# Kernel optimization log

Hardware: AMD Instinct MI355X
Metric: run time of the kernel (lower is better)

The kernel has to match this reference:

```python
import jax, jax.numpy as jnp
import numpy as np

B, S, D, H = 1, 4096, 1024, 16
DH = D // H  # 64
SCALE = D ** 0.5  # original divides by input_dim**0.5, not head_dim**0.5


def setup_inputs() -> dict:
    key = jax.random.key(0)
    ks = jax.random.split(key, 11)
    s = lambda i, shape, sc=1.0: jax.random.normal(ks[i], shape, dtype=jnp.float32) * sc
    w_init = 1.0 / np.sqrt(D)
    return {
        "q": s(0, (B, S, D)),
        "k": s(1, (B, S, D)),
        "v": s(2, (B, S, D)),
        "Wq": s(3, (H, D, DH), w_init),
        "bq": jnp.zeros((H, DH), jnp.float32),
        "Wk": s(4, (H, D, DH), w_init),
        "bk": jnp.zeros((H, DH), jnp.float32),
        "Wv": s(5, (H, D, DH), w_init),
        "bv": jnp.zeros((H, DH), jnp.float32),
        "Wo": s(6, (D, D), w_init),
        "bo": jnp.zeros((D,), jnp.float32),
    }


def reference(q, k, v, Wq, bq, Wk, bk, Wv, bv, Wo, bo):
    # Per-head Dense projections, batched over heads: [B,S,D] x [H,D,dh] -> [B,H,S,dh]
    Q = jnp.einsum("bsd,hde->bhse", q, Wq) + bq[None, :, None, :]
    K = jnp.einsum("bsd,hde->bhse", k, Wk) + bk[None, :, None, :]
    V = jnp.einsum("bsd,hde->bhse", v, Wv) + bv[None, :, None, :]
    # Scaled dot-product attention; note scale = sqrt(input_dim) as in source
    scores = jnp.einsum("bhse,bhte->bhst", Q, K) / SCALE  # [B,H,S,S]
    attn = jax.nn.softmax(scores, axis=-1)
    out = jnp.einsum("bhst,bhte->bhse", attn, V)  # [B,H,S,dh]
    # Concat heads along feature dim (head order matches the Python loop)
    concat = out.transpose(0, 2, 1, 3).reshape(q.shape[0], q.shape[1], H * DH)
    return concat @ Wo + bo
```

## Files before the change

### kernel.cpp

```cpp
#include <hip/hip_runtime.h>
#include <hip/hip_bf16.h>

#define S_LEN 4096
#define D_MODEL 1024
#define NH 16
#define DHEAD 64
#define QSCALE 0.0450843293f

typedef __attribute__((ext_vector_type(8))) short short8;
typedef __attribute__((ext_vector_type(4))) float floatx4;

__device__ __forceinline__ unsigned short f2bf(float f) {
    unsigned int x = __float_as_uint(f);
    x += 0x7fffu + ((x >> 16) & 1u);
    return (unsigned short)(x >> 16);
}

__device__ __forceinline__ float exp2_fast(float x) {
    return __builtin_amdgcn_exp2f(x);
}

__device__ __forceinline__ void async_copy16(const unsigned short* g, unsigned short* l) {
    __builtin_amdgcn_global_load_lds(
        (const __attribute__((address_space(1))) void*)g,
        (__attribute__((address_space(3))) void*)l, 16, 0, 0);
}

__global__ __launch_bounds__(256) void prep_all(
    const float* __restrict__ q, const float* __restrict__ k,
    const float* __restrict__ v,
    const float* __restrict__ Wq, const float* __restrict__ Wk,
    const float* __restrict__ Wv, const float* __restrict__ Wo,
    unsigned short* __restrict__ dst, unsigned short* __restrict__ ws)
{
    __shared__ float L[64][65];
    const int tid = threadIdx.x;

    if (blockIdx.x < 6144) {
        long i = (long)(blockIdx.x * 256 + tid) * 8;
        int which = (int)(i >> 22);
        long off = i & ((1 << 22) - 1);
        const float* src = (which == 0) ? q : (which == 1) ? k : v;
        float4 f0 = *(const float4*)&src[off];
        float4 f1 = *(const float4*)&src[off + 4];
        uint4 o;
        o.x = (unsigned int)f2bf(f0.x) | ((unsigned int)f2bf(f0.y) << 16);
        o.y = (unsigned int)f2bf(f0.z) | ((unsigned int)f2bf(f0.w) << 16);
        o.z = (unsigned int)f2bf(f1.x) | ((unsigned int)f2bf(f1.y) << 16);
        o.w = (unsigned int)f2bf(f1.z) | ((unsigned int)f2bf(f1.w) << 16);
        *(uint4*)&dst[i] = o;
        return;
    }

    const int bx  = blockIdx.x - 6144;
    const int mat = bx >> 8;

    if (mat < 3) {
        const float* W = (mat == 0) ? Wq : (mat == 1) ? Wk : Wv;
        unsigned short* WT = ws + (size_t)mat * (1u << 20);
        int h  = (bx >> 4) & 15;
        int dt = bx & 15;
        #pragma unroll
        for (int i = 0; i < 16; i++) {
            int idx = i * 256 + tid;
            int dp = idx >> 6, e = idx & 63;
            L[e][dp] = W[h * 65536 + (dt * 64 + dp) * 64 + e];
        }
        __syncthreads();
        #pragma unroll
        for (int i = 0; i < 16; i++) {
            int idx = i * 256 + tid;
            int e = idx >> 6, dp = idx & 63;
            WT[(h * 64 + e) * 1024 + dt * 64 + dp] = f2bf(L[e][dp]);
        }
    } else {
        unsigned short* WoT = ws + (size_t)3 * (1u << 20);
        int rt = (bx >> 4) & 15;
        int ct = bx & 15;
        #pragma unroll
        for (int i = 0; i < 16; i++) {
            int idx = i * 256 + tid;
            int dp = idx >> 6, np = idx & 63;
            L[np][dp] = Wo[(rt * 64 + dp) * 1024 + ct * 64 + np];
        }
        __syncthreads();
        #pragma unroll
        for (int i = 0; i < 16; i++) {
            int idx = i * 256 + tid;
            int np = idx >> 6, dp = idx & 63;
            WoT[(ct * 64 + np) * 1024 + rt * 64 + dp] = f2bf(L[np][dp]);
        }
    }
}

#define GEMM_CORE(XPTR, WPTR)                                                   \
    for (int k0 = 0; k0 < D_MODEL; k0 += 64) {                                  \
        __syncthreads();                                                        \
        _Pragma("unroll")                                                       \
        for (int i = 0; i < 4; i++) {                                           \
            async_copy16(&XPTR[(size_t)(m0 + srow + i * 8) * D_MODEL + k0 + scol], \
                         &As[(wave * 32 + i * 8) * 64]);                        \
            async_copy16(&WPTR[(size_t)(n0 + srow + i * 8) * D_MODEL + k0 + scol], \
                         &Bs[(wave * 32 + i * 8) * 64]);                        \
        }                                                                       \
        __syncthreads();                                                        \
        _Pragma("unroll")                                                       \
        for (int ks = 0; ks < 2; ks++) {                                        \
            short8 af[4], bf[4];                                                \
            _Pragma("unroll")                                                   \
            for (int i = 0; i < 4; i++)                                         \
                af[i] = *(const short8*)&As[(wr * 64 + i * 16 + m) * 64 + ks * 32 + quad * 8]; \
            _Pragma("unroll")                                                   \
            for (int j = 0; j < 4; j++)                                         \
                bf[j] = *(const short8*)&Bs[(wc * 64 + j * 16 + m) * 64 + ks * 32 + quad * 8]; \
            _Pragma("unroll")                                                   \
            for (int i = 0; i < 4; i++) {                                       \
                _Pragma("unroll")                                               \
                for (int j = 0; j < 4; j++)                                     \
                    acc[i][j] = __builtin_amdgcn_mfma_f32_16x16x32_bf16(af[i], bf[j], acc[i][j], 0, 0, 0); \
            }                                                                   \
        }                                                                       \
    }

__global__ __launch_bounds__(256) void qkv_gemm(
    const unsigned short* __restrict__ Xbase, const unsigned short* __restrict__ WTbase,
    const float* __restrict__ bq, const float* __restrict__ bk,
    const float* __restrict__ bv,
    unsigned short* __restrict__ Qbuf, unsigned short* __restrict__ Kbuf,
    unsigned short* __restrict__ Vbuf)
{
    __shared__ __align__(16) unsigned short AB[2 * 128 * 64];
    unsigned short* As = AB;
    unsigned short* Bs = AB + 128 * 64;

    const int z = blockIdx.z;
    const unsigned short* X  = Xbase + (size_t)z * (4u << 20);
    const unsigned short* WT = WTbase + (size_t)z * (1u << 20);
    const float* bias = (z == 0) ? bq : (z == 1) ? bk : bv;

    const int n0 = blockIdx.x * 128;
    const int m0 = blockIdx.y * 128;
    const int tid = threadIdx.x, wave = tid >> 6, lane = tid & 63;
    const int m = lane & 15, quad = lane >> 4;
    const int wr = wave >> 1, wc = wave & 1;
    const int srow = wave * 32 + (lane >> 3);
    const int scol = (lane & 7) * 8;

    floatx4 acc[4][4];
    #pragma unroll
    for (int i = 0; i < 4; i++)
        #pragma unroll
        for (int j = 0; j < 4; j++) acc[i][j] = (floatx4){0.f, 0.f, 0.f, 0.f};

    GEMM_CORE(X, WT)

    if (z == 2) {
        #pragma unroll
        for (int j = 0; j < 4; j++) {
            int n = n0 + wc * 64 + j * 16 + m;
            int h = n >> 6, e = n & 63;
            float bvv = bias[n];
            #pragma unroll
            for (int i = 0; i < 4; i++) {
                int sbase = m0 + wr * 64 + i * 16 + quad * 4;
                ushort4 pk;
                pk.x = f2bf(acc[i][j][0] + bvv);
                pk.y = f2bf(acc[i][j][1] + bvv);
                pk.z = f2bf(acc[i][j][2] + bvv);
                pk.w = f2bf(acc[i][j][3] + bvv);
                *(ushort4*)&Vbuf[h * (DHEAD * S_LEN) + e * S_LEN + sbase] = pk;
            }
        }
        return;
    }

    const float scale = (z == 0) ? QSCALE : 1.0f;
    unsigned short* outp = (z == 0) ? Qbuf : Kbuf;
    __syncthreads();
    unsigned short* stage = wc ? Bs : As;
    #pragma unroll
    for (int j = 0; j < 4; j++) {
        int e = j * 16 + m;
        float bvv = bias[n0 + wc * 64 + e];
        #pragma unroll
        for (int i = 0; i < 4; i++) {
            int rbase = wr * 64 + i * 16 + quad * 4;
            #pragma unroll
            for (int r = 0; r < 4; r++) {
                int rowl = rbase + r;
                stage[rowl * 64 + (e ^ ((rowl & 7) << 3))] =
                    f2bf((acc[i][j][r] + bvv) * scale);
            }
        }
    }
    __syncthreads();
    const int h0 = n0 >> 6;
    const size_t base0 = (size_t)h0 * (S_LEN * DHEAD) + (size_t)m0 * DHEAD;
    const size_t base1 = base0 + (size_t)(S_LEN * DHEAD);
    #pragma unroll
    for (int s = 0; s < 4; s++) {
        int o = tid * 8 + s * 2048;
        int row = o >> 6, c0 = o & 63;
        int cs = c0 ^ ((row & 7) << 3);
        *(uint4*)&outp[base0 + o] = *(const uint4*)&As[row * 64 + cs];
        *(uint4*)&outp[base1 + o] = *(const uint4*)&Bs[row * 64 + cs];
    }
}

__global__ __launch_bounds__(256) void out_gemm(
    const unsigned short* __restrict__ Cbuf, const unsigned short* __restrict__ WoT,
    const float* __restrict__ bo, float* __restrict__ out)
{
    __shared__ __align__(16) unsigned short AB[2 * 128 * 64];
    unsigned short* As = AB;
    unsigned short* Bs = AB + 128 * 64;

    const int n0 = blockIdx.x * 128;
    const int m0 = blockIdx.y * 128;
    const int tid = threadIdx.x, wave = tid >> 6, lane = tid & 63;
    const int m = lane & 15, quad = lane >> 4;
    const int wr = wave >> 1, wc = wave & 1;
    const int srow = wave * 32 + (lane >> 3);
    const int scol = (lane & 7) * 8;

    floatx4 acc[4][4];
    #pragma unroll
    for (int i = 0; i < 4; i++)
        #pragma unroll
        for (int j = 0; j < 4; j++) acc[i][j] = (floatx4){0.f, 0.f, 0.f, 0.f};

    GEMM_CORE(Cbuf, WoT)

    __syncthreads();
    float* Fs = (float*)AB;
    #pragma unroll
    for (int half = 0; half < 2; half++) {
        if (wr == half) {
            #pragma unroll
            for (int j = 0; j < 4; j++) {
                int c = wc * 64 + j * 16 + m;
                float bvv = bo[n0 + c];
                #pragma unroll
                for (int i = 0; i < 4; i++) {
                    int rbase = i * 16 + quad * 4;
                    #pragma unroll
                    for (int r = 0; r < 4; r++) {
                        int rowl = rbase + r;
                        Fs[rowl * 128 + (c ^ ((rowl & 7) << 2))] = acc[i][j][r] + bvv;
                    }
                }
            }
        }
        __syncthreads();
        #pragma unroll
        for (int s = 0; s < 8; s++) {
            int o = tid * 4 + s * 1024;
            int row = o >> 7, c0 = o & 127;
            int cs = c0 ^ ((row & 7) << 2);
            *(float4*)&out[(size_t)(m0 + half * 64 + row) * D_MODEL + n0 + c0] =
                *(const float4*)&Fs[row * 128 + cs];
        }
        __syncthreads();
    }
}

__global__ __launch_bounds__(512) void attn_kernel(
    const unsigned short* __restrict__ Q, const unsigned short* __restrict__ K,
    const unsigned short* __restrict__ VT, unsigned short* __restrict__ concat)
{
    __shared__ __align__(16) unsigned char ldsraw[49152];
    unsigned short* lds16 = (unsigned short*)ldsraw;

    const int h  = blockIdx.y;
    const int q0 = blockIdx.x * 128;
    const unsigned short* Qh = Q  + h * (S_LEN * DHEAD);
    const unsigned short* Kh = K  + h * (S_LEN * DHEAD);
    const unsigned short* Vh = VT + h * (DHEAD * S_LEN);

    const int tid  = threadIdx.x;
    const int wave = tid >> 6;
    const int wt   = wave & 3;
    const int wq   = wave >> 2;
    const int lane = tid & 63;
    const int m    = lane & 15;
    const int quad = lane >> 4;
    const int swz  = (m & 7) << 3;
    const int lrow = lane >> 3;
    const int lcol = ((lane & 7) * 8) ^ (lrow << 3);

    unsigned short* Ps = lds16 + 16384;

    #pragma unroll
    for (int i = 0; i < 2; i++) {
        int c = 2 * wave + i;
        async_copy16(&Qh[(size_t)(q0 + 8 * c + lrow) * DHEAD + lcol], Ps + c * 512);
    }
    async_copy16(&Kh[(size_t)(8 * wave + lrow) * DHEAD + lcol], lds16 + wave * 512);
    async_copy16(&Vh[(size_t)(8 * wave + lrow) * S_LEN + lcol], lds16 + 8192 + wave * 512);
    asm volatile("s_waitcnt vmcnt(0)" ::: "memory");
    __builtin_amdgcn_s_barrier();

    short8 bq[4][2];
    #pragma unroll
    for (int qc = 0; qc < 4; qc++)
        #pragma unroll
        for (int ks = 0; ks < 2; ks++)
            bq[qc][ks] = *(const short8*)&Ps[(wq * 64 + qc * 16 + m) * 64 + ((ks * 32 + quad * 8) ^ swz)];
    __syncthreads();

    short8 vone;
    #pragma unroll
    for (int i = 0; i < 8; i++) vone[i] = (short)0x3F80;

    floatx4 O[4];
    #pragma unroll
    for (int nb = 0; nb < 4; nb++) O[nb] = (floatx4){0.f, 0.f, 0.f, 0.f};
    floatx4 Lacc = (floatx4){0.f, 0.f, 0.f, 0.f};

    for (int t0 = 0; t0 < S_LEN; t0 += 64) {
        const int cur = (t0 >> 6) & 1;
        unsigned short* Ksc = lds16 + cur * 4096;
        unsigned short* Vsc = lds16 + 8192 + cur * 4096;

        if (t0) {
            asm volatile("s_waitcnt vmcnt(0)" ::: "memory");
            __builtin_amdgcn_s_barrier();
        }
        if (t0 + 64 < S_LEN) {
            unsigned short* Ksn = lds16 + (cur ^ 1) * 4096;
            unsigned short* Vsn = lds16 + 8192 + (cur ^ 1) * 4096;
            async_copy16(&Kh[(size_t)(t0 + 64 + 8 * wave + lrow) * DHEAD + lcol],
                         Ksn + wave * 512);
            async_copy16(&Vh[(size_t)(8 * wave + lrow) * S_LEN + t0 + 64 + lcol],
                         Vsn + wave * 512);
        }

        floatx4 st[4];
        #pragma unroll
        for (int qc = 0; qc < 4; qc++) st[qc] = (floatx4){0.f, 0.f, 0.f, 0.f};
        #pragma unroll
        for (int ks = 0; ks < 2; ks++) {
            short8 a = *(const short8*)&Ksc[(wt * 16 + m) * 64 + ((ks * 32 + quad * 8) ^ swz)];
            __builtin_amdgcn_s_setprio(1);
            #pragma unroll
            for (int qc = 0; qc < 4; qc++)
                st[qc] = __builtin_amdgcn_mfma_f32_16x16x32_bf16(a, bq[qc][ks], st[qc], 0, 0, 0);
            __builtin_amdgcn_s_setprio(0);
        }

        #pragma unroll
        for (int qc = 0; qc < 4; qc++) {
            float p0 = exp2_fast(st[qc][0]);
            float p1 = exp2_fast(st[qc][1]);
            float p2 = exp2_fast(st[qc][2]);
            float p3 = exp2_fast(st[qc][3]);
            unsigned r0, r1;
            asm("v_cvt_pk_bf16_f32 %0, %1, %2" : "=v"(r0) : "v"(p0), "v"(p1));
            asm("v_cvt_pk_bf16_f32 %0, %1, %2" : "=v"(r1) : "v"(p2), "v"(p3));
            uint2 pk;
            pk.x = r0;
            pk.y = r1;
            *(uint2*)&Ps[(wq * 64 + qc * 16 + m) * 64 + ((wt * 16 + quad * 4) ^ swz)] = pk;
        }
        asm volatile("s_waitcnt lgkmcnt(0)" ::: "memory");
        __builtin_amdgcn_s_barrier();

        #pragma unroll
        for (int ks = 0; ks < 2; ks++) {
            short8 ap = *(const short8*)&Ps[(wave * 16 + m) * 64 + ((ks * 32 + quad * 8) ^ swz)];
            __builtin_amdgcn_s_setprio(1);
            #pragma unroll
            for (int nb = 0; nb < 4; nb++) {
                short8 bv = *(const short8*)&Vsc[(nb * 16 + m) * 64 + ((ks * 32 + quad * 8) ^ swz)];
                O[nb] = __builtin_amdgcn_mfma_f32_16x16x32_bf16(ap, bv, O[nb], 0, 0, 0);
            }
            Lacc = __builtin_amdgcn_mfma_f32_16x16x32_bf16(ap, vone, Lacc, 0, 0, 0);
            __builtin_amdgcn_s_setprio(0);
        }
    }

    float linv[4];
    #pragma unroll
    for (int r = 0; r < 4; r++) linv[r] = 1.0f / Lacc[r];

    #pragma unroll
    for (int nb = 0; nb < 4; nb++) {
        int e = nb * 16 + m;
        #pragma unroll
        for (int r = 0; r < 4; r++) {
            int s = q0 + wave * 16 + quad * 4 + r;
            concat[s * D_MODEL + h * DHEAD + e] = f2bf(O[nb][r] * linv[r]);
        }
    }
}

extern "C" void kernel_launch(void* const* d_in, const int* in_sizes, int n_in,
                              void* d_out, int out_size, void* d_ws, size_t ws_size,
                              hipStream_t stream) {
    const float* q  = (const float*)d_in[0];
    const float* k  = (const float*)d_in[1];
    const float* v  = (const float*)d_in[2];
    const float* Wq = (const float*)d_in[3];
    const float* bq = (const float*)d_in[4];
    const float* Wk = (const float*)d_in[5];
    const float* bk = (const float*)d_in[6];
    const float* Wv = (const float*)d_in[7];
    const float* bv = (const float*)d_in[8];
    const float* Wo = (const float*)d_in[9];
    const float* bo = (const float*)d_in[10];
    float* out = (float*)d_out;

    unsigned short* ws = (unsigned short*)d_ws;
    const size_t M1 = 1u << 20;
    unsigned short* WqT  = ws;
    unsigned short* WoT  = ws + 3 * M1;
    unsigned short* Qbuf = ws + 4 * M1;
    unsigned short* Kbuf = ws + 8 * M1;
    unsigned short* Vbuf = ws + 12 * M1;
    unsigned short* Cbuf = ws + 16 * M1;
    unsigned short* qb   = ws + 20 * M1;

    prep_all<<<7168, 256, 0, stream>>>(q, k, v, Wq, Wk, Wv, Wo, qb, ws);

    dim3 gq(8, 32, 3);
    qkv_gemm<<<gq, 256, 0, stream>>>(qb, WqT, bq, bk, bv, Qbuf, Kbuf, Vbuf);

    dim3 ga(32, 16);
    attn_kernel<<<ga, 512, 0, stream>>>(Qbuf, Kbuf, Vbuf, Cbuf);

    dim3 gg(8, 32);
    out_gemm<<<gg, 256, 0, stream>>>(Cbuf, WoT, bo, out);
}
```

Baseline: 271.9 us.

## Double-buffer GEMM LDS loads and double the attention query tile per block

The shared GEMM core now prefetches the next K-slice into a second LDS buffer while MFMAs run on the current one, and raises wave priority around the MFMA bursts. This replaces two barriers per iteration with one and is meant to hide global-load latency. The attention kernel now handles 256 queries per block instead of 128, halving the grid, so each K/V tile loaded into LDS is reused across twice as many queries. The cost is more registers and LDS per block, which lowers occupancy, and only 256 attention blocks run on a large GPU.

```diff
diff --git a/kernel.cpp b/kernel.cpp
--- a/kernel.cpp
+++ b/kernel.cpp
@@ -94,32 +94,50 @@
 }
 
 #define GEMM_CORE(XPTR, WPTR)                                                   \
+    _Pragma("unroll")                                                           \
+    for (int i = 0; i < 4; i++) {                                               \
+        async_copy16(&XPTR[(size_t)(m0 + srow + i * 8) * D_MODEL + scol],       \
+                     &LB[(wave * 32 + i * 8) * 64]);                            \
+        async_copy16(&WPTR[(size_t)(n0 + srow + i * 8) * D_MODEL + scol],       \
+                     &LB[16384 + (wave * 32 + i * 8) * 64]);                    \
+    }                                                                           \
+    asm volatile("s_waitcnt vmcnt(0)" ::: "memory");                            \
+    __builtin_amdgcn_s_barrier();                                               \
     for (int k0 = 0; k0 < D_MODEL; k0 += 64) {                                  \
-        __syncthreads();                                                        \
-        _Pragma("unroll")                                                       \
-        for (int i = 0; i < 4; i++) {                                           \
-            async_copy16(&XPTR[(size_t)(m0 + srow + i * 8) * D_MODEL + k0 + scol], \
-                         &As[(wave * 32 + i * 8) * 64]);                        \
-            async_copy16(&WPTR[(size_t)(n0 + srow + i * 8) * D_MODEL + k0 + scol], \
-                         &Bs[(wave * 32 + i * 8) * 64]);                        \
+        const int cb = (k0 >> 6) & 1;                                           \
+        const unsigned short* Ac = LB + cb * 8192;                              \
+        const unsigned short* Bc = LB + 16384 + cb * 8192;                      \
+        if (k0 + 64 < D_MODEL) {                                                \
+            unsigned short* An = LB + (cb ^ 1) * 8192;                          \
+            unsigned short* Bn = LB + 16384 + (cb ^ 1) * 8192;                  \
+            _Pragma("unroll")                                                   \
+            for (int i = 0; i < 4; i++) {                                       \
+                async_copy16(&XPTR[(size_t)(m0 + srow + i * 8) * D_MODEL + k0 + 64 + scol], \
+                             &An[(wave * 32 + i * 8) * 64]);                    \
+                async_copy16(&WPTR[(size_t)(n0 + srow + i * 8) * D_MODEL + k0 + 64 + scol], \
+                             &Bn[(wave * 32 + i * 8) * 64]);                    \
+            }                                                                   \
         }                                                                       \
-        __syncthreads();                                                        \
         _Pragma("unroll")                                                       \
         for (int ks = 0; ks < 2; ks++) {                                        \
             short8 af[4], bf[4];                                                \
             _Pragma("unroll")                                                   \
             for (int i = 0; i < 4; i++)                                         \
-                af[i] = *(const short8*)&As[(wr * 64 + i * 16 + m) * 64 + ks * 32 + quad * 8]; \
+                af[i] = *(const short8*)&Ac[(wr * 64 + i * 16 + m) * 64 + ks * 32 + quad * 8]; \
             _Pragma("unroll")                                                   \
             for (int j = 0; j < 4; j++)                                         \
-                bf[j] = *(const short8*)&Bs[(wc * 64 + j * 16 + m) * 64 + ks * 32 + quad * 8]; \
+                bf[j] = *(const short8*)&Bc[(wc * 64 + j * 16 + m) * 64 + ks * 32 + quad * 8]; \
+            __builtin_amdgcn_s_setprio(1);                                      \
             _Pragma("unroll")                                                   \
             for (int i = 0; i < 4; i++) {                                       \
                 _Pragma("unroll")                                               \
                 for (int j = 0; j < 4; j++)                                     \
                     acc[i][j] = __builtin_amdgcn_mfma_f32_16x16x32_bf16(af[i], bf[j], acc[i][j], 0, 0, 0); \
             }                                                                   \
+            __builtin_amdgcn_s_setprio(0);                                      \
         }                                                                       \
+        asm volatile("s_waitcnt vmcnt(0)" ::: "memory");                        \
+        __builtin_amdgcn_s_barrier();                                           \
     }
 
 __global__ __launch_bounds__(256) void qkv_gemm(
@@ -129,9 +147,7 @@
     unsigned short* __restrict__ Qbuf, unsigned short* __restrict__ Kbuf,
     unsigned short* __restrict__ Vbuf)
 {
-    __shared__ __align__(16) unsigned short AB[2 * 128 * 64];
-    unsigned short* As = AB;
-    unsigned short* Bs = AB + 128 * 64;
+    __shared__ __align__(16) unsigned short LB[32768];
 
     const int z = blockIdx.z;
     const unsigned short* X  = Xbase + (size_t)z * (4u << 20);
@@ -177,7 +193,7 @@
     const float scale = (z == 0) ? QSCALE : 1.0f;
     unsigned short* outp = (z == 0) ? Qbuf : Kbuf;
     __syncthreads();
-    unsigned short* stage = wc ? Bs : As;
+    unsigned short* stage = LB + (wc ? 8192 : 0);
     #pragma unroll
     for (int j = 0; j < 4; j++) {
         int e = j * 16 + m;
@@ -202,8 +218,8 @@
         int o = tid * 8 + s * 2048;
         int row = o >> 6, c0 = o & 63;
         int cs = c0 ^ ((row & 7) << 3);
-        *(uint4*)&outp[base0 + o] = *(const uint4*)&As[row * 64 + cs];
-        *(uint4*)&outp[base1 + o] = *(const uint4*)&Bs[row * 64 + cs];
+        *(uint4*)&outp[base0 + o] = *(const uint4*)&LB[row * 64 + cs];
+        *(uint4*)&outp[base1 + o] = *(const uint4*)&LB[8192 + row * 64 + cs];
     }
 }
 
@@ -211,9 +227,7 @@
     const unsigned short* __restrict__ Cbuf, const unsigned short* __restrict__ WoT,
     const float* __restrict__ bo, float* __restrict__ out)
 {
-    __shared__ __align__(16) unsigned short AB[2 * 128 * 64];
-    unsigned short* As = AB;
-    unsigned short* Bs = AB + 128 * 64;
+    __shared__ __align__(16) unsigned short LB[32768];
 
     const int n0 = blockIdx.x * 128;
     const int m0 = blockIdx.y * 128;
@@ -232,7 +246,7 @@
     GEMM_CORE(Cbuf, WoT)
 
     __syncthreads();
-    float* Fs = (float*)AB;
+    float* Fs = (float*)LB;
     #pragma unroll
     for (int half = 0; half < 2; half++) {
         if (wr == half) {
@@ -268,11 +282,11 @@
     const unsigned short* __restrict__ Q, const unsigned short* __restrict__ K,
     const unsigned short* __restrict__ VT, unsigned short* __restrict__ concat)
 {
-    __shared__ __align__(16) unsigned char ldsraw[49152];
+    __shared__ __align__(16) unsigned char ldsraw[65536];
     unsigned short* lds16 = (unsigned short*)ldsraw;
 
     const int h  = blockIdx.y;
-    const int q0 = blockIdx.x * 128;
+    const int q0 = blockIdx.x * 256;
     const unsigned short* Qh = Q  + h * (S_LEN * DHEAD);
     const unsigned short* Kh = K  + h * (S_LEN * DHEAD);
     const unsigned short* Vh = VT + h * (DHEAD * S_LEN);
@@ -280,7 +294,7 @@
     const int tid  = threadIdx.x;
     const int wave = tid >> 6;
     const int wt   = wave & 3;
-    const int wq   = wave >> 2;
+    const int wq2  = wave >> 2;
     const int lane = tid & 63;
     const int m    = lane & 15;
     const int quad = lane >> 4;
@@ -291,8 +305,8 @@
     unsigned short* Ps = lds16 + 16384;
 
     #pragma unroll
-    for (int i = 0; i < 2; i++) {
-        int c = 2 * wave + i;
+    for (int i = 0; i < 4; i++) {
+        int c = 4 * wave + i;
         async_copy16(&Qh[(size_t)(q0 + 8 * c + lrow) * DHEAD + lcol], Ps + c * 512);
     }
     async_copy16(&Kh[(size_t)(8 * wave + lrow) * DHEAD + lcol], lds16 + wave * 512);
@@ -300,22 +314,26 @@
     asm volatile("s_waitcnt vmcnt(0)" ::: "memory");
     __builtin_amdgcn_s_barrier();
 
-    short8 bq[4][2];
-    #pragma unroll
-    for (int qc = 0; qc < 4; qc++)
+    short8 bq[8][2];
+    #pragma unroll
+    for (int qc = 0; qc < 8; qc++)
         #pragma unroll
         for (int ks = 0; ks < 2; ks++)
-            bq[qc][ks] = *(const short8*)&Ps[(wq * 64 + qc * 16 + m) * 64 + ((ks * 32 + quad * 8) ^ swz)];
+            bq[qc][ks] = *(const short8*)&Ps[(wq2 * 128 + qc * 16 + m) * 64 + ((ks * 32 + quad * 8) ^ swz)];
     __syncthreads();
 
     short8 vone;
     #pragma unroll
     for (int i = 0; i < 8; i++) vone[i] = (short)0x3F80;
 
-    floatx4 O[4];
-    #pragma unroll
-    for (int nb = 0; nb < 4; nb++) O[nb] = (floatx4){0.f, 0.f, 0.f, 0.f};
-    floatx4 Lacc = (floatx4){0.f, 0.f, 0.f, 0.f};
+    floatx4 O[2][4];
+    #pragma unroll
+    for (int mi = 0; mi < 2; mi++)
+        #pragma unroll
+        for (int nb = 0; nb < 4; nb++) O[mi][nb] = (floatx4){0.f, 0.f, 0.f, 0.f};
+    floatx4 Lacc[2];
+    Lacc[0] = (floatx4){0.f, 0.f, 0.f, 0.f};
+    Lacc[1] = (floatx4){0.f, 0.f, 0.f, 0.f};
 
     for (int t0 = 0; t0 < S_LEN; t0 += 64) {
         const int cur = (t0 >> 6) & 1;
@@ -335,21 +353,21 @@
                          Vsn + wave * 512);
         }
 
-        floatx4 st[4];
-        #pragma unroll
-        for (int qc = 0; qc < 4; qc++) st[qc] = (floatx4){0.f, 0.f, 0.f, 0.f};
+        floatx4 st[8];
+        #pragma unroll
+        for (int qc = 0; qc < 8; qc++) st[qc] = (floatx4){0.f, 0.f, 0.f, 0.f};
         #pragma unroll
         for (int ks = 0; ks < 2; ks++) {
             short8 a = *(const short8*)&Ksc[(wt * 16 + m) * 64 + ((ks * 32 + quad * 8) ^ swz)];
             __builtin_amdgcn_s_setprio(1);
             #pragma unroll
-            for (int qc = 0; qc < 4; qc++)
+            for (int qc = 0; qc < 8; qc++)
                 st[qc] = __builtin_amdgcn_mfma_f32_16x16x32_bf16(a, bq[qc][ks], st[qc], 0, 0, 0);
             __builtin_amdgcn_s_setprio(0);
         }
 
         #pragma unroll
-        for (int qc = 0; qc < 4; qc++) {
+        for (int qc = 0; qc < 8; qc++) {
             float p0 = exp2_fast(st[qc][0]);
             float p1 = exp2_fast(st[qc][1]);
             float p2 = exp2_fast(st[qc][2]);
@@ -360,36 +378,41 @@
             uint2 pk;
             pk.x = r0;
             pk.y = r1;
-            *(uint2*)&Ps[(wq * 64 + qc * 16 + m) * 64 + ((wt * 16 + quad * 4) ^ swz)] = pk;
+            *(uint2*)&Ps[(wq2 * 128 + qc * 16 + m) * 64 + ((wt * 16 + quad * 4) ^ swz)] = pk;
         }
         asm volatile("s_waitcnt lgkmcnt(0)" ::: "memory");
         __builtin_amdgcn_s_barrier();
 
         #pragma unroll
         for (int ks = 0; ks < 2; ks++) {
-            short8 ap = *(const short8*)&Ps[(wave * 16 + m) * 64 + ((ks * 32 + quad * 8) ^ swz)];
+            short8 ap0 = *(const short8*)&Ps[(wave * 32 + m) * 64 + ((ks * 32 + quad * 8) ^ swz)];
+            short8 ap1 = *(const short8*)&Ps[(wave * 32 + 16 + m) * 64 + ((ks * 32 + quad * 8) ^ swz)];
             __builtin_amdgcn_s_setprio(1);
             #pragma unroll
             for (int nb = 0; nb < 4; nb++) {
                 short8 bv = *(const short8*)&Vsc[(nb * 16 + m) * 64 + ((ks * 32 + quad * 8) ^ swz)];
-                O[nb] = __builtin_amdgcn_mfma_f32_16x16x32_bf16(ap, bv, O[nb], 0, 0, 0);
+                O[0][nb] = __builtin_amdgcn_mfma_f32_16x16x32_bf16(ap0, bv, O[0][nb], 0, 0, 0);
+                O[1][nb] = __builtin_amdgcn_mfma_f32_16x16x32_bf16(ap1, bv, O[1][nb], 0, 0, 0);
             }
-            Lacc = __builtin_amdgcn_mfma_f32_16x16x32_bf16(ap, vone, Lacc, 0, 0, 0);
+            Lacc[0] = __builtin_amdgcn_mfma_f32_16x16x32_bf16(ap0, vone, Lacc[0], 0, 0, 0);
+            Lacc[1] = __builtin_amdgcn_mfma_f32_16x16x32_bf16(ap1, vone, Lacc[1], 0, 0, 0);
             __builtin_amdgcn_s_setprio(0);
         }
     }
 
-    float linv[4];
-    #pragma unroll
-    for (int r = 0; r < 4; r++) linv[r] = 1.0f / Lacc[r];
-
-    #pragma unroll
-    for (int nb = 0; nb < 4; nb++) {
-        int e = nb * 16 + m;
-        #pragma unroll
-        for (int r = 0; r < 4; r++) {
-            int s = q0 + wave * 16 + quad * 4 + r;
-            concat[s * D_MODEL + h * DHEAD + e] = f2bf(O[nb][r] * linv[r]);
+    #pragma unroll
+    for (int mi = 0; mi < 2; mi++) {
+        float linv[4];
+        #pragma unroll
+        for (int r = 0; r < 4; r++) linv[r] = 1.0f / Lacc[mi][r];
+        #pragma unroll
+        for (int nb = 0; nb < 4; nb++) {
+            int e = nb * 16 + m;
+            #pragma unroll
+            for (int r = 0; r < 4; r++) {
+                int s = q0 + wave * 32 + mi * 16 + quad * 4 + r;
+                concat[s * D_MODEL + h * DHEAD + e] = f2bf(O[mi][nb][r] * linv[r]);
+            }
         }
     }
 }
@@ -425,7 +448,7 @@
     dim3 gq(8, 32, 3);
     qkv_gemm<<<gq, 256, 0, stream>>>(qb, WqT, bq, bk, bv, Qbuf, Kbuf, Vbuf);
 
-    dim3 ga(32, 16);
+    dim3 ga(16, 16);
     attn_kernel<<<ga, 512, 0, stream>>>(Qbuf, Kbuf, Vbuf, Cbuf);
 
     dim3 gg(8, 32);
```

Measured after the change: 258.8 us. -4.8%, faster.
